# Kernel tuning notes

Measured on AMD Instinct MI355X. Metric: run time of the kernel, lower is better.

## Reference

```python
import jax, jax.numpy as jnp
import numpy as np

N = 65536      # nodes in batched graph
E = 2097152    # edges (avg degree 32)
V = 1000       # chord vocabulary size
F_IN = 128     # chord feature dim
H = 256        # hidden_dim
OUT = 128      # out_dim
G = 256        # number of graphs in batch


def _gcn_layer(x, W, b, row, col, norm, n):
    # x: [n, f_in] -> [n, f_out]; PyG GCNConv: linear then normalized aggregation + bias
    x = x @ W
    msg = x[row] * norm[:, None]            # gather at source, scale by sym-norm
    return jax.ops.segment_sum(msg, col, num_segments=n) + b


def setup_inputs() -> dict:
    key = jax.random.key(0)
    ks = jax.random.split(key, 9)
    chord_feats = jax.random.normal(ks[0], (V, F_IN), jnp.float32)
    W1 = jax.random.normal(ks[1], (F_IN, H), jnp.float32) * 0.05
    b1 = jnp.zeros((H,), jnp.float32)
    W2 = jax.random.normal(ks[2], (H, OUT), jnp.float32) * 0.05
    b2 = jnp.zeros((OUT,), jnp.float32)
    edge_attr = jax.random.uniform(ks[3], (E,), jnp.float32)          # positive edge weights
    node_indices = jax.random.randint(ks[4], (N,), 0, V, jnp.int64)
    edge_index = jax.random.randint(ks[5], (2, E), 0, N, jnp.int64)
    batch_index = jnp.sort(jax.random.randint(ks[6], (N,), 0, G, jnp.int64))
    return {"chord_feats": chord_feats, "W1": W1, "b1": b1, "W2": W2, "b2": b2,
            "edge_attr": edge_attr, "node_indices": node_indices,
            "edge_index": edge_index, "batch_index": batch_index}


def reference(chord_feats, W1, b1, W2, b2, edge_attr, node_indices, edge_index, batch_index):
    loops = jnp.arange(N, dtype=edge_index.dtype)
    row = jnp.concatenate([edge_index[0], loops])   # source
    col = jnp.concatenate([edge_index[1], loops])   # target
    ew = jnp.concatenate([edge_attr, jnp.ones((N,), edge_attr.dtype)])  # self-loop weight 1
    # symmetric GCN normalization: D^-1/2 A D^-1/2
    deg = jax.ops.segment_sum(ew, col, num_segments=N)
    dis = jnp.where(deg > 0, jax.lax.rsqrt(jnp.maximum(deg, 1e-30)), 0.0)
    norm = dis[row] * ew * dis[col]

    x = chord_feats[node_indices]                   # [N, F_IN]
    x = jax.nn.relu(_gcn_layer(x, W1, b1, row, col, norm, N))
    x = jax.nn.relu(_gcn_layer(x, W2, b2, row, col, norm, N))

    # global_mean_pool over batch_index
    sums = jax.ops.segment_sum(x, batch_index, num_segments=G)
    counts = jax.ops.segment_sum(jnp.ones((N,), x.dtype), batch_index, num_segments=G)
    return sums / jnp.maximum(counts, 1.0)[:, None]
```

## Files before the change

### kernel.cpp

```cpp
#include <hip/hip_runtime.h>
#include <hip/hip_fp16.h>
#include <math.h>

constexpr int N_NODES = 65536;
constexpr int N_EDGES = 2097152;
constexpr int F_IN    = 128;
constexpr int H_DIM   = 256;
constexpr int O_DIM   = 128;
constexpr int N_GRAPH = 256;
constexpr int V_SIZE  = 1000;

constexpr int EPB  = 8192;
constexpr int NBLK = N_EDGES / EPB;
constexpr float FXP = 16777216.0f;

typedef _Float16 half8 __attribute__((ext_vector_type(8)));
typedef float floatx4 __attribute__((ext_vector_type(4)));


__global__ void k_init(float* __restrict__ pool, const int* __restrict__ batch,
                       float* __restrict__ cntf, const float* __restrict__ cf,
                       const float* __restrict__ W1, __half* __restrict__ cfW1,
                       const float* __restrict__ W2, _Float16* __restrict__ W2T) {
    __shared__ float xs[8 * F_IN];
    int i = blockIdx.x * blockDim.x + threadIdx.x;
    if (i < N_GRAPH * O_DIM) pool[i] = 0.0f;
    if (blockIdx.x == 0) {
        int g = threadIdx.x;
        int lo = 0, hi = N_NODES;
        while (lo < hi) { int m = (lo + hi) >> 1; if (batch[m] < g) lo = m + 1; else hi = m; }
        int start = lo;
        lo = 0; hi = N_NODES;
        while (lo < hi) { int m = (lo + hi) >> 1; if (batch[m] <= g) lo = m + 1; else hi = m; }
        cntf[g] = (float)(lo - start);
    }
    if (blockIdx.x < V_SIZE / 8) {
        int rb = blockIdx.x * 8;
        int t  = threadIdx.x;
        #pragma unroll
        for (int p = 0; p < 4; ++p) {
            int idx = p * 256 + t;
            int r = idx >> 7, k = idx & 127;
            xs[idx] = cf[(size_t)(rb + r) * F_IN + k];
        }
        __syncthreads();
        float acc[8] = {};
        for (int k = 0; k < F_IN; ++k) {
            float w = W1[k * H_DIM + t];
            #pragma unroll
            for (int j = 0; j < 8; ++j) acc[j] += xs[j * F_IN + k] * w;
        }
        #pragma unroll
        for (int j = 0; j < 8; ++j)
            cfW1[(size_t)(rb + j) * H_DIM + t] = __float2half(acc[j]);
    }
    if (blockIdx.x >= 128) {
        int idx = (blockIdx.x - 128) * 256 + threadIdx.x;
        int nn = idx >> 8, kk = idx & 255;
        W2T[idx] = (_Float16)W2[kk * O_DIM + nn];
    }
}


__global__ void k_hist(const int* __restrict__ col, int* __restrict__ hist) {
    __shared__ int h[256];
    int t = threadIdx.x;
    h[t] = 0;
    __syncthreads();
    int base = blockIdx.x * EPB;
    #pragma unroll
    for (int i = 0; i < EPB / 256; ++i)
        atomicAdd(&h[col[base + i * 256 + t] >> 8], 1);
    __syncthreads();
    hist[t * NBLK + blockIdx.x] = h[t];
}


__global__ void k_scan1(const int* __restrict__ in, int* __restrict__ out,
                        int* __restrict__ bsum) {
    __shared__ int s[256];
    int tid = threadIdx.x;
    int i = blockIdx.x * 256 + tid;
    int v = in[i];
    s[tid] = v;
    __syncthreads();
    for (int d = 1; d < 256; d <<= 1) {
        int t = (tid >= d) ? s[tid - d] : 0;
        __syncthreads();
        s[tid] += t;
        __syncthreads();
    }
    out[i] = s[tid] - v;
    if (tid == 255) bsum[blockIdx.x] = s[255];
}

__global__ void k_scan2(int* __restrict__ bsum) {
    __shared__ int s[256];
    int tid = threadIdx.x;
    int v = bsum[tid];
    s[tid] = v;
    __syncthreads();
    for (int d = 1; d < 256; d <<= 1) {
        int t = (tid >= d) ? s[tid - d] : 0;
        __syncthreads();
        s[tid] += t;
        __syncthreads();
    }
    bsum[tid] = s[tid] - v;
}


__global__ void k_part(const int* __restrict__ row, const int* __restrict__ col,
                       const float* __restrict__ ew, const int* __restrict__ nidx,
                       const int* __restrict__ hoffs, const int* __restrict__ bsum,
                       int2* __restrict__ part) {
    __shared__ int cur[256];
    int t = threadIdx.x;
    cur[t] = hoffs[t * NBLK + blockIdx.x] + bsum[t];
    __syncthreads();
    int base = blockIdx.x * EPB;
    for (int i = 0; i < EPB / 256; ++i) {
        int e = base + i * 256 + t;
        int r = row[e], c = col[e];
        unsigned hw = (unsigned)__half_as_ushort(__float2half(ew[e]));
        int vb = nidx[r];
        int slot = atomicAdd(&cur[c >> 8], 1);
        int2 rec;
        rec.x = (r << 16) | ((c & 255) << 8) | (vb >> 2);
        rec.y = (int)(((unsigned)(vb & 3) << 16) | hw);
        part[slot] = rec;
    }
}


__global__ void k_build1(const int* __restrict__ hoffs, const int* __restrict__ bsum,
                         const int2* __restrict__ part, float* __restrict__ dis,
                         int* __restrict__ offs) {
    __shared__ unsigned long long dc[256];
    __shared__ int sc[256];
    int t = threadIdx.x;
    int bucket = blockIdx.x;
    dc[t] = 0ULL;
    __syncthreads();
    int start = hoffs[bucket * NBLK] + bsum[bucket];
    int end   = (bucket == 255) ? N_EDGES : (hoffs[(bucket + 1) * NBLK] + bsum[bucket + 1]);
    for (int j = start + t; j < end; j += 256) {
        int2 rec = part[j];
        int dst = (rec.x >> 8) & 255;
        float w = __half2float(__ushort_as_half((unsigned short)(rec.y & 0xFFFF)));
        atomicAdd(&dc[dst], (1ULL << 40) |
                  (unsigned long long)(unsigned)(w * FXP + 0.5f));
    }
    __syncthreads();
    unsigned long long v = dc[t];
    float deg = 1.0f + (float)(v & 0xFFFFFFFFFFULL) * (1.0f / FXP);
    dis[bucket * 256 + t] = 1.0f / sqrtf(deg);
    int cnt = (int)(v >> 40);
    sc[t] = cnt;
    __syncthreads();
    for (int d = 1; d < 256; d <<= 1) {
        int x = (t >= d) ? sc[t - d] : 0;
        __syncthreads();
        sc[t] += x;
        __syncthreads();
    }
    offs[bucket * 256 + t] = start + sc[t] - cnt;
    if (bucket == 255 && t == 255) offs[N_NODES] = N_EDGES;
}


__global__ void k_build2(const int* __restrict__ hoffs, const int* __restrict__ bsum,
                         const int2* __restrict__ part, const float* __restrict__ dis,
                         const int* __restrict__ offs, int2* __restrict__ csr) {
    __shared__ int cur[256];
    int t = threadIdx.x;
    int bucket = blockIdx.x;
    cur[t] = offs[bucket * 256 + t];
    __syncthreads();
    int start = hoffs[bucket * NBLK] + bsum[bucket];
    int end   = (bucket == 255) ? N_EDGES : (hoffs[(bucket + 1) * NBLK] + bsum[bucket + 1]);
    for (int j = start + t; j < end; j += 256) {
        int2 rec = part[j];
        int dst = (rec.x >> 8) & 255;
        unsigned src = ((unsigned)rec.x) >> 16;
        int vb = ((rec.x & 255) << 2) | ((rec.y >> 16) & 3);
        float w = __half2float(__ushort_as_half((unsigned short)(rec.y & 0xFFFF)));
        float nm = dis[src] * w;
        int slot = atomicAdd(&cur[dst], 1);
        int2 e;
        e.x = (int)((src << 10) | (unsigned)vb);
        e.y = __float_as_int(nm);
        csr[slot] = e;
    }
}

__device__ __forceinline__ void acc8(float* e, int4 v, float n) {
    float2 f0 = __half22float2(*(__half2*)&v.x);
    float2 f1 = __half22float2(*(__half2*)&v.y);
    float2 f2 = __half22float2(*(__half2*)&v.z);
    float2 f3 = __half22float2(*(__half2*)&v.w);
    e[0] += f0.x * n; e[1] += f0.y * n;
    e[2] += f1.x * n; e[3] += f1.y * n;
    e[4] += f2.x * n; e[5] += f2.y * n;
    e[6] += f3.x * n; e[7] += f3.y * n;
}


__global__ void k_agg1(const int4* __restrict__ cfW1, const int* __restrict__ nidx,
                       const float* __restrict__ dis, const int* __restrict__ offs,
                       const int2* __restrict__ csr, const float4* __restrict__ b1f4,
                       int4* __restrict__ h1) {
    int wave = threadIdx.x >> 6;
    int lane = threadIdx.x & 63;
    int g    = lane >> 5;
    int sl   = lane & 31;
    int c = blockIdx.x * 4 + wave;
    float d = dis[c];
    int4 sp = cfW1[(size_t)nidx[c] * 32 + sl];
    float esum[8] = {0.f, 0.f, 0.f, 0.f, 0.f, 0.f, 0.f, 0.f};
    int a0 = offs[c], a1 = offs[c + 1];
    int s = a0;
    if (s < a1 && (s & 1)) {
        int sb = __builtin_amdgcn_readfirstlane(s);
        int2 e0 = csr[sb];
        int4 v0 = cfW1[(size_t)(e0.x & 1023) * 32 + sl];
        float n = (g == 0) ? __int_as_float(e0.y) : 0.0f;
        acc8(esum, v0, n);
        ++s;
    }
    for (; s + 8 <= a1; s += 8) {
        int sb = __builtin_amdgcn_readfirstlane(s);
        int4 ee[4];
        #pragma unroll
        for (int u = 0; u < 4; ++u) ee[u] = *(const int4*)(csr + sb + 2 * u);
        int4 v[4]; float n[4];
        #pragma unroll
        for (int u = 0; u < 4; ++u) {
            int ex = g ? ee[u].z : ee[u].x;
            int ey = g ? ee[u].w : ee[u].y;
            n[u] = __int_as_float(ey);
            v[u] = cfW1[(size_t)(ex & 1023) * 32 + sl];
        }
        #pragma unroll
        for (int u = 0; u < 4; ++u) acc8(esum, v[u], n[u]);
    }
    for (; s + 2 <= a1; s += 2) {
        int sb = __builtin_amdgcn_readfirstlane(s);
        int4 ee = *(const int4*)(csr + sb);
        int ex = g ? ee.z : ee.x;
        int ey = g ? ee.w : ee.y;
        int4 v0 = cfW1[(size_t)(ex & 1023) * 32 + sl];
        acc8(esum, v0, __int_as_float(ey));
    }
    if (s < a1) {
        int sb = __builtin_amdgcn_readfirstlane(s);
        int2 e0 = csr[sb];
        int4 v0 = cfW1[(size_t)(e0.x & 1023) * 32 + sl];
        float n = (g == 0) ? __int_as_float(e0.y) : 0.0f;
        acc8(esum, v0, n);
    }
    #pragma unroll
    for (int k = 0; k < 8; ++k) esum[k] += __shfl_xor(esum[k], 32, 64);

    float dd = d * d;
    float2 s0 = __half22float2(*(__half2*)&sp.x);
    float2 s1 = __half22float2(*(__half2*)&sp.y);
    float2 s2 = __half22float2(*(__half2*)&sp.z);
    float2 s3 = __half22float2(*(__half2*)&sp.w);
    float4 bb0 = b1f4[2 * sl];
    float4 bb1 = b1f4[2 * sl + 1];
    float r[8];
    r[0] = bb0.x + s0.x * dd + d * esum[0];
    r[1] = bb0.y + s0.y * dd + d * esum[1];
    r[2] = bb0.z + s1.x * dd + d * esum[2];
    r[3] = bb0.w + s1.y * dd + d * esum[3];
    r[4] = bb1.x + s2.x * dd + d * esum[4];
    r[5] = bb1.y + s2.y * dd + d * esum[5];
    r[6] = bb1.z + s3.x * dd + d * esum[6];
    r[7] = bb1.w + s3.y * dd + d * esum[7];
    #pragma unroll
    for (int k = 0; k < 8; ++k) r[k] = r[k] > 0.f ? r[k] : 0.f;
    float2 p0 = {r[0], r[1]}, p1 = {r[2], r[3]}, p2 = {r[4], r[5]}, p3 = {r[6], r[7]};
    __half2 h0 = __float22half2_rn(p0);
    __half2 h1v = __float22half2_rn(p1);
    __half2 h2 = __float22half2_rn(p2);
    __half2 h3 = __float22half2_rn(p3);
    int4 outv;
    outv.x = *(int*)&h0;
    outv.y = *(int*)&h1v;
    outv.z = *(int*)&h2;
    outv.w = *(int*)&h3;
    if (lane < 32) h1[(size_t)c * 32 + sl] = outv;
}


__global__ void k_gemm2(const _Float16* __restrict__ h1, const _Float16* __restrict__ W2T,
                        __half* __restrict__ xw2h) {
    int wave = threadIdx.x >> 6;
    int lane = threadIdx.x & 63;
    int quad = lane >> 4;
    int n    = lane & 15;
    int tm   = blockIdx.x * 4 + wave;
    const _Float16* arow = h1 + (size_t)(tm * 16 + n) * H_DIM;
    half8 a[8];
    #pragma unroll
    for (int kt = 0; kt < 8; ++kt)
        a[kt] = *(const half8*)(arow + kt * 32 + quad * 8);
    #pragma unroll
    for (int nt = 0; nt < 8; ++nt) {
        floatx4 acc = {0.f, 0.f, 0.f, 0.f};
        const _Float16* brow = W2T + (size_t)(nt * 16 + n) * H_DIM;
        #pragma unroll
        for (int kt = 0; kt < 8; ++kt) {
            half8 b = *(const half8*)(brow + kt * 32 + quad * 8);
            acc = __builtin_amdgcn_mfma_f32_16x16x32_f16(a[kt], b, acc, 0, 0, 0);
        }
        #pragma unroll
        for (int r = 0; r < 4; ++r) {
            int rowi = tm * 16 + quad * 4 + r;
            xw2h[(size_t)rowi * O_DIM + nt * 16 + n] = __float2half(acc[r]);
        }
    }
}


__global__ void k_agg2_pool(const int4* __restrict__ xw2h, const float* __restrict__ b2,
                            const float* __restrict__ dis, const int* __restrict__ offs,
                            const int2* __restrict__ csr, const int* __restrict__ batch,
                            float* __restrict__ pool) {
    __shared__ float red[4][128];
    __shared__ int bgs[4];
    int wave = threadIdx.x >> 6;
    int lane = threadIdx.x & 63;
    int grp  = lane >> 4;
    int sl   = lane & 15;
    int c = blockIdx.x * 4 + wave;
    float d = dis[c];
    int4 sp = xw2h[(size_t)c * 16 + sl];
    float esum[8] = {0.f, 0.f, 0.f, 0.f, 0.f, 0.f, 0.f, 0.f};
    int s0 = offs[c], s1 = offs[c + 1];
    int s = s0;
    for (; s + 16 <= s1; s += 16) {
        int sb = __builtin_amdgcn_readfirstlane(s);
        int2 e[4];
        #pragma unroll
        for (int u = 0; u < 4; ++u) e[u] = csr[sb + 4 * u + grp];
        int4 v[4];
        #pragma unroll
        for (int u = 0; u < 4; ++u)
            v[u] = xw2h[(size_t)(((unsigned)e[u].x) >> 10) * 16 + sl];
        #pragma unroll
        for (int u = 0; u < 4; ++u) acc8(esum, v[u], __int_as_float(e[u].y));
    }
    for (; s + 4 <= s1; s += 4) {
        int sb = __builtin_amdgcn_readfirstlane(s);
        int2 e0 = csr[sb + grp];
        int4 v0 = xw2h[(size_t)(((unsigned)e0.x) >> 10) * 16 + sl];
        acc8(esum, v0, __int_as_float(e0.y));
    }
    if (s < s1) {
        int sb = __builtin_amdgcn_readfirstlane(s);
        int idx = sb + grp;
        int idc = idx < s1 ? idx : s1 - 1;
        int2 e0 = csr[idc];
        int4 v0 = xw2h[(size_t)(((unsigned)e0.x) >> 10) * 16 + sl];
        float n = (idx < s1) ? __int_as_float(e0.y) : 0.0f;
        acc8(esum, v0, n);
    }
    #pragma unroll
    for (int k = 0; k < 8; ++k) {
        esum[k] += __shfl_xor(esum[k], 16, 64);
        esum[k] += __shfl_xor(esum[k], 32, 64);
    }
    float dd = d * d;
    float2 f0 = __half22float2(*(__half2*)&sp.x);
    float2 f1 = __half22float2(*(__half2*)&sp.y);
    float2 f2 = __half22float2(*(__half2*)&sp.z);
    float2 f3 = __half22float2(*(__half2*)&sp.w);
    float4 bb0 = ((const float4*)b2)[2 * sl];
    float4 bb1 = ((const float4*)b2)[2 * sl + 1];
    float acc[8];
    acc[0] = bb0.x + f0.x * dd + d * esum[0];
    acc[1] = bb0.y + f0.y * dd + d * esum[1];
    acc[2] = bb0.z + f1.x * dd + d * esum[2];
    acc[3] = bb0.w + f1.y * dd + d * esum[3];
    acc[4] = bb1.x + f2.x * dd + d * esum[4];
    acc[5] = bb1.y + f2.y * dd + d * esum[5];
    acc[6] = bb1.z + f3.x * dd + d * esum[6];
    acc[7] = bb1.w + f3.y * dd + d * esum[7];
    #pragma unroll
    for (int k = 0; k < 8; ++k) acc[k] = acc[k] > 0.f ? acc[k] : 0.f;
    if (grp == 0) {
        #pragma unroll
        for (int k = 0; k < 8; ++k) red[wave][8 * sl + k] = acc[k];
    }
    if (lane == 0) bgs[wave] = batch[c];
    __syncthreads();
    if (wave == 0) {
        float2 a;
        a.x = red[0][2 * lane];
        a.y = red[0][2 * lane + 1];
        int cg = bgs[0];
        #pragma unroll
        for (int w = 1; w < 4; ++w) {
            int g = bgs[w];
            float2 r;
            r.x = red[w][2 * lane];
            r.y = red[w][2 * lane + 1];
            if (g == cg) { a.x += r.x; a.y += r.y; }
            else {
                atomicAdd(&pool[cg * O_DIM + 2 * lane], a.x);
                atomicAdd(&pool[cg * O_DIM + 2 * lane + 1], a.y);
                a = r; cg = g;
            }
        }
        atomicAdd(&pool[cg * O_DIM + 2 * lane], a.x);
        atomicAdd(&pool[cg * O_DIM + 2 * lane + 1], a.y);
    }
}

__global__ void k_final(const float* __restrict__ pool, const float* __restrict__ cnt,
                        float* __restrict__ out) {
    int t = blockIdx.x * blockDim.x + threadIdx.x;
    if (t < N_GRAPH * O_DIM) {
        int g = t / O_DIM;
        out[t] = pool[t] / fmaxf(cnt[g], 1.0f);
    }
}


extern "C" void kernel_launch(void* const* d_in, const int* in_sizes, int n_in,
                              void* d_out, int out_size, void* d_ws, size_t ws_size,
                              hipStream_t stream) {
    const float* cf   = (const float*)d_in[0];
    const float* W1   = (const float*)d_in[1];
    const float* b1   = (const float*)d_in[2];
    const float* W2   = (const float*)d_in[3];
    const float* b2   = (const float*)d_in[4];
    const float* ew   = (const float*)d_in[5];
    const int*   nidx = (const int*)d_in[6];
    const int*   eidx = (const int*)d_in[7];
    const int*   bidx = (const int*)d_in[8];
    float* out = (float*)d_out;

    const int* row = eidx;
    const int* col = eidx + N_EDGES;

    char* ws = (char*)d_ws;
    size_t off = 0;
    int*   hist  = (int*)  (ws + off); off += (size_t)N_NODES * 4;
    int*   hoffs = (int*)  (ws + off); off += (size_t)N_NODES * 4;
    int*   bsum  = (int*)  (ws + off); off += 4096;
    float* dis   = (float*)(ws + off); off += (size_t)N_NODES * 4;
    int*   offs  = (int*)  (ws + off); off += (size_t)(N_NODES + 16) * 4;
    int2*  csr   = (int2*) (ws + off); off += (size_t)N_EDGES * 8;
    float* pool  = (float*)(ws + off); off += (size_t)(N_GRAPH * O_DIM + N_GRAPH) * 4;
    __half* cfW1 = (__half*)(ws + off); off += (size_t)V_SIZE * H_DIM * 2;
    _Float16* W2T = (_Float16*)(ws + off); off += (size_t)O_DIM * H_DIM * 2;
    off = (off + 255) & ~(size_t)255;
    int2*  part  = (int2*) (ws + off); off += (size_t)N_EDGES * 8;
    __half* h1   = (__half*)(ws + off);
    __half* xw2h = (__half*)part;
    float* cntf  = pool + N_GRAPH * O_DIM;

    k_init<<<256, 256, 0, stream>>>(pool, bidx, cntf, cf, W1, cfW1, W2, W2T);
    k_hist<<<NBLK, 256, 0, stream>>>(col, hist);
    k_scan1<<<256, 256, 0, stream>>>(hist, hoffs, bsum);
    k_scan2<<<1, 256, 0, stream>>>(bsum);

    k_part<<<NBLK, 256, 0, stream>>>(row, col, ew, nidx, hoffs, bsum, part);
    k_build1<<<256, 256, 0, stream>>>(hoffs, bsum, part, dis, offs);
    k_build2<<<256, 256, 0, stream>>>(hoffs, bsum, part, dis, offs, csr);

    k_agg1<<<N_NODES / 4, 256, 0, stream>>>((const int4*)cfW1, nidx, dis, offs, csr,
                                            (const float4*)b1, (int4*)h1);

    k_gemm2<<<N_NODES / 64, 256, 0, stream>>>((const _Float16*)h1, W2T, xw2h);
    k_agg2_pool<<<N_NODES / 4, 256, 0, stream>>>((const int4*)xw2h, b2, dis, offs, csr,
                                                 bidx, pool);

    k_final<<<(N_GRAPH * O_DIM + 255) / 256, 256, 0, stream>>>(pool, cntf, out);
}
```

Measured before the change: 331.5 us.

## Split layer-2 aggregation into four feature-slice passes with sliced xw2h layout

The GEMM2 output is stored as four column slices of 32 halves per node, and the aggregation-plus-pool kernel runs four passes, each gathering only a 64-byte slice per neighbor with 16 edges handled per wave step. The aim is to shrink each pass's gather working set so it fits better in cache and gives better locality for random neighbor reads. The cost is reading the CSR edge list four times, plus more cross-lane shuffles and more pool atomics. CSR loads are marked nontemporal so these repeated streams do not evict the feature slices.

```diff
diff --git a/kernel.cpp b/kernel.cpp
--- a/kernel.cpp
+++ b/kernel.cpp
@@ -318,7 +318,9 @@
         #pragma unroll
         for (int r = 0; r < 4; ++r) {
             int rowi = tm * 16 + quad * 4 + r;
-            xw2h[(size_t)rowi * O_DIM + nt * 16 + n] = __float2half(acc[r]);
+            int dgl = nt * 16 + n;
+            xw2h[(size_t)(dgl >> 5) * ((size_t)N_NODES * 32)
+                 + (size_t)rowi * 32 + (dgl & 31)] = __float2half(acc[r]);
         }
     }
 }
@@ -328,94 +330,94 @@
                             const float* __restrict__ dis, const int* __restrict__ offs,
                             const int2* __restrict__ csr, const int* __restrict__ batch,
                             float* __restrict__ pool) {
-    __shared__ float red[4][128];
+    __shared__ float red[4][32];
     __shared__ int bgs[4];
     int wave = threadIdx.x >> 6;
     int lane = threadIdx.x & 63;
-    int grp  = lane >> 4;
-    int sl   = lane & 15;
-    int c = blockIdx.x * 4 + wave;
+    int grp  = lane >> 2;
+    int sl   = lane & 3;
+    int pass = blockIdx.x >> 14;
+    int c    = (blockIdx.x & 16383) * 4 + wave;
+    const int4* t = xw2h + (size_t)pass * N_NODES * 4;
     float d = dis[c];
-    int4 sp = xw2h[(size_t)c * 16 + sl];
+    int4 sp = t[(size_t)c * 4 + sl];
     float esum[8] = {0.f, 0.f, 0.f, 0.f, 0.f, 0.f, 0.f, 0.f};
     int s0 = offs[c], s1 = offs[c + 1];
     int s = s0;
+    for (; s + 32 <= s1; s += 32) {
+        int sb = __builtin_amdgcn_readfirstlane(s);
+        long long r0 = __builtin_nontemporal_load((const long long*)(csr + sb + grp));
+        long long r1 = __builtin_nontemporal_load((const long long*)(csr + sb + 16 + grp));
+        int2 e0 = *(int2*)&r0;
+        int2 e1 = *(int2*)&r1;
+        int4 v0 = t[(size_t)(((unsigned)e0.x) >> 10) * 4 + sl];
+        int4 v1 = t[(size_t)(((unsigned)e1.x) >> 10) * 4 + sl];
+        acc8(esum, v0, __int_as_float(e0.y));
+        acc8(esum, v1, __int_as_float(e1.y));
+    }
     for (; s + 16 <= s1; s += 16) {
         int sb = __builtin_amdgcn_readfirstlane(s);
-        int2 e[4];
-        #pragma unroll
-        for (int u = 0; u < 4; ++u) e[u] = csr[sb + 4 * u + grp];
-        int4 v[4];
-        #pragma unroll
-        for (int u = 0; u < 4; ++u)
-            v[u] = xw2h[(size_t)(((unsigned)e[u].x) >> 10) * 16 + sl];
-        #pragma unroll
-        for (int u = 0; u < 4; ++u) acc8(esum, v[u], __int_as_float(e[u].y));
-    }
-    for (; s + 4 <= s1; s += 4) {
-        int sb = __builtin_amdgcn_readfirstlane(s);
-        int2 e0 = csr[sb + grp];
-        int4 v0 = xw2h[(size_t)(((unsigned)e0.x) >> 10) * 16 + sl];
+        long long r0 = __builtin_nontemporal_load((const long long*)(csr + sb + grp));
+        int2 e0 = *(int2*)&r0;
+        int4 v0 = t[(size_t)(((unsigned)e0.x) >> 10) * 4 + sl];
         acc8(esum, v0, __int_as_float(e0.y));
     }
     if (s < s1) {
         int sb = __builtin_amdgcn_readfirstlane(s);
         int idx = sb + grp;
         int idc = idx < s1 ? idx : s1 - 1;
-        int2 e0 = csr[idc];
-        int4 v0 = xw2h[(size_t)(((unsigned)e0.x) >> 10) * 16 + sl];
+        long long r0 = __builtin_nontemporal_load((const long long*)(csr + idc));
+        int2 e0 = *(int2*)&r0;
+        int4 v0 = t[(size_t)(((unsigned)e0.x) >> 10) * 4 + sl];
         float n = (idx < s1) ? __int_as_float(e0.y) : 0.0f;
         acc8(esum, v0, n);
     }
     #pragma unroll
     for (int k = 0; k < 8; ++k) {
+        esum[k] += __shfl_xor(esum[k], 4, 64);
+        esum[k] += __shfl_xor(esum[k], 8, 64);
         esum[k] += __shfl_xor(esum[k], 16, 64);
         esum[k] += __shfl_xor(esum[k], 32, 64);
     }
-    float dd = d * d;
-    float2 f0 = __half22float2(*(__half2*)&sp.x);
-    float2 f1 = __half22float2(*(__half2*)&sp.y);
-    float2 f2 = __half22float2(*(__half2*)&sp.z);
-    float2 f3 = __half22float2(*(__half2*)&sp.w);
-    float4 bb0 = ((const float4*)b2)[2 * sl];
-    float4 bb1 = ((const float4*)b2)[2 * sl + 1];
-    float acc[8];
-    acc[0] = bb0.x + f0.x * dd + d * esum[0];
-    acc[1] = bb0.y + f0.y * dd + d * esum[1];
-    acc[2] = bb0.z + f1.x * dd + d * esum[2];
-    acc[3] = bb0.w + f1.y * dd + d * esum[3];
-    acc[4] = bb1.x + f2.x * dd + d * esum[4];
-    acc[5] = bb1.y + f2.y * dd + d * esum[5];
-    acc[6] = bb1.z + f3.x * dd + d * esum[6];
-    acc[7] = bb1.w + f3.y * dd + d * esum[7];
-    #pragma unroll
-    for (int k = 0; k < 8; ++k) acc[k] = acc[k] > 0.f ? acc[k] : 0.f;
     if (grp == 0) {
-        #pragma unroll
-        for (int k = 0; k < 8; ++k) red[wave][8 * sl + k] = acc[k];
+        float dd = d * d;
+        float2 f0 = __half22float2(*(__half2*)&sp.x);
+        float2 f1 = __half22float2(*(__half2*)&sp.y);
+        float2 f2 = __half22float2(*(__half2*)&sp.z);
+        float2 f3 = __half22float2(*(__half2*)&sp.w);
+        float4 bb0 = ((const float4*)b2)[pass * 8 + sl * 2];
+        float4 bb1 = ((const float4*)b2)[pass * 8 + sl * 2 + 1];
+        float acc[8];
+        acc[0] = bb0.x + f0.x * dd + d * esum[0];
+        acc[1] = bb0.y + f0.y * dd + d * esum[1];
+        acc[2] = bb0.z + f1.x * dd + d * esum[2];
+        acc[3] = bb0.w + f1.y * dd + d * esum[3];
+        acc[4] = bb1.x + f2.x * dd + d * esum[4];
+        acc[5] = bb1.y + f2.y * dd + d * esum[5];
+        acc[6] = bb1.z + f3.x * dd + d * esum[6];
+        acc[7] = bb1.w + f3.y * dd + d * esum[7];
+        #pragma unroll
+        for (int k = 0; k < 8; ++k) {
+            float v = acc[k] > 0.f ? acc[k] : 0.f;
+            red[wave][sl * 8 + k] = v;
+        }
     }
     if (lane == 0) bgs[wave] = batch[c];
     __syncthreads();
-    if (wave == 0) {
-        float2 a;
-        a.x = red[0][2 * lane];
-        a.y = red[0][2 * lane + 1];
+    if (wave == 0 && lane < 32) {
+        float a = red[0][lane];
         int cg = bgs[0];
         #pragma unroll
         for (int w = 1; w < 4; ++w) {
             int g = bgs[w];
-            float2 r;
-            r.x = red[w][2 * lane];
-            r.y = red[w][2 * lane + 1];
-            if (g == cg) { a.x += r.x; a.y += r.y; }
+            float r = red[w][lane];
+            if (g == cg) { a += r; }
             else {
-                atomicAdd(&pool[cg * O_DIM + 2 * lane], a.x);
-                atomicAdd(&pool[cg * O_DIM + 2 * lane + 1], a.y);
+                atomicAdd(&pool[cg * O_DIM + pass * 32 + lane], a);
                 a = r; cg = g;
             }
         }
-        atomicAdd(&pool[cg * O_DIM + 2 * lane], a.x);
-        atomicAdd(&pool[cg * O_DIM + 2 * lane + 1], a.y);
+        atomicAdd(&pool[cg * O_DIM + pass * 32 + lane], a);
     }
 }
 
@@ -476,8 +478,8 @@
                                             (const float4*)b1, (int4*)h1);
 
     k_gemm2<<<N_NODES / 64, 256, 0, stream>>>((const _Float16*)h1, W2T, xw2h);
-    k_agg2_pool<<<N_NODES / 4, 256, 0, stream>>>((const int4*)xw2h, b2, dis, offs, csr,
-                                                 bidx, pool);
+    k_agg2_pool<<<4 * (N_NODES / 4), 256, 0, stream>>>((const int4*)xw2h, b2, dis, offs,
+                                                       csr, bidx, pool);
 
     k_final<<<(N_GRAPH * O_DIM + 255) / 256, 256, 0, stream>>>(pool, cntf, out);
 }
```

Measured after the change: 390.1 us. +17.7%, slower.

## Fuse layer-1 aggregation with layer-2 GEMM via LDS; deepen agg2 unroll

Applied to the files above, without the earlier changes.

Merges the layer-1 aggregation kernel and the layer-2 MFMA GEMM into one kernel. Each block aggregates 16 nodes into an LDS tile and then multiplies that tile by W2T, with each wave covering two output column tiles. This removes the global h1 write and reread and one kernel launch. The trade-off is that each wave now handles 4 nodes serially and the grid is 4x smaller, which may reduce latency hiding. Separately, the agg2 edge loop is unrolled from 16 to 32 edges with nontemporal CSR loads, to put more loads in flight.

```diff
diff --git a/kernel.cpp b/kernel.cpp
--- a/kernel.cpp
+++ b/kernel.cpp
@@ -206,108 +206,110 @@
 }
 
 
-__global__ void k_agg1(const int4* __restrict__ cfW1, const int* __restrict__ nidx,
-                       const float* __restrict__ dis, const int* __restrict__ offs,
-                       const int2* __restrict__ csr, const float4* __restrict__ b1f4,
-                       int4* __restrict__ h1) {
+__global__ void __launch_bounds__(256) k_agg1g2(
+        const int4* __restrict__ cfW1, const int* __restrict__ nidx,
+        const float* __restrict__ dis, const int* __restrict__ offs,
+        const int2* __restrict__ csr, const float4* __restrict__ b1f4,
+        const _Float16* __restrict__ W2T, __half* __restrict__ xw2h) {
+    __shared__ _Float16 h1s[16 * 264];
     int wave = threadIdx.x >> 6;
     int lane = threadIdx.x & 63;
     int g    = lane >> 5;
     int sl   = lane & 31;
-    int c = blockIdx.x * 4 + wave;
-    float d = dis[c];
-    int4 sp = cfW1[(size_t)nidx[c] * 32 + sl];
-    float esum[8] = {0.f, 0.f, 0.f, 0.f, 0.f, 0.f, 0.f, 0.f};
-    int a0 = offs[c], a1 = offs[c + 1];
-    int s = a0;
-    if (s < a1 && (s & 1)) {
-        int sb = __builtin_amdgcn_readfirstlane(s);
-        int2 e0 = csr[sb];
-        int4 v0 = cfW1[(size_t)(e0.x & 1023) * 32 + sl];
-        float n = (g == 0) ? __int_as_float(e0.y) : 0.0f;
-        acc8(esum, v0, n);
-        ++s;
-    }
-    for (; s + 8 <= a1; s += 8) {
-        int sb = __builtin_amdgcn_readfirstlane(s);
-        int4 ee[4];
-        #pragma unroll
-        for (int u = 0; u < 4; ++u) ee[u] = *(const int4*)(csr + sb + 2 * u);
-        int4 v[4]; float n[4];
-        #pragma unroll
-        for (int u = 0; u < 4; ++u) {
-            int ex = g ? ee[u].z : ee[u].x;
-            int ey = g ? ee[u].w : ee[u].y;
-            n[u] = __int_as_float(ey);
-            v[u] = cfW1[(size_t)(ex & 1023) * 32 + sl];
-        }
-        #pragma unroll
-        for (int u = 0; u < 4; ++u) acc8(esum, v[u], n[u]);
-    }
-    for (; s + 2 <= a1; s += 2) {
-        int sb = __builtin_amdgcn_readfirstlane(s);
-        int4 ee = *(const int4*)(csr + sb);
-        int ex = g ? ee.z : ee.x;
-        int ey = g ? ee.w : ee.y;
-        int4 v0 = cfW1[(size_t)(ex & 1023) * 32 + sl];
-        acc8(esum, v0, __int_as_float(ey));
-    }
-    if (s < a1) {
-        int sb = __builtin_amdgcn_readfirstlane(s);
-        int2 e0 = csr[sb];
-        int4 v0 = cfW1[(size_t)(e0.x & 1023) * 32 + sl];
-        float n = (g == 0) ? __int_as_float(e0.y) : 0.0f;
-        acc8(esum, v0, n);
-    }
-    #pragma unroll
-    for (int k = 0; k < 8; ++k) esum[k] += __shfl_xor(esum[k], 32, 64);
-
-    float dd = d * d;
-    float2 s0 = __half22float2(*(__half2*)&sp.x);
-    float2 s1 = __half22float2(*(__half2*)&sp.y);
-    float2 s2 = __half22float2(*(__half2*)&sp.z);
-    float2 s3 = __half22float2(*(__half2*)&sp.w);
+    int rowbase = blockIdx.x * 16;
+
     float4 bb0 = b1f4[2 * sl];
     float4 bb1 = b1f4[2 * sl + 1];
-    float r[8];
-    r[0] = bb0.x + s0.x * dd + d * esum[0];
-    r[1] = bb0.y + s0.y * dd + d * esum[1];
-    r[2] = bb0.z + s1.x * dd + d * esum[2];
-    r[3] = bb0.w + s1.y * dd + d * esum[3];
-    r[4] = bb1.x + s2.x * dd + d * esum[4];
-    r[5] = bb1.y + s2.y * dd + d * esum[5];
-    r[6] = bb1.z + s3.x * dd + d * esum[6];
-    r[7] = bb1.w + s3.y * dd + d * esum[7];
-    #pragma unroll
-    for (int k = 0; k < 8; ++k) r[k] = r[k] > 0.f ? r[k] : 0.f;
-    float2 p0 = {r[0], r[1]}, p1 = {r[2], r[3]}, p2 = {r[4], r[5]}, p3 = {r[6], r[7]};
-    __half2 h0 = __float22half2_rn(p0);
-    __half2 h1v = __float22half2_rn(p1);
-    __half2 h2 = __float22half2_rn(p2);
-    __half2 h3 = __float22half2_rn(p3);
-    int4 outv;
-    outv.x = *(int*)&h0;
-    outv.y = *(int*)&h1v;
-    outv.z = *(int*)&h2;
-    outv.w = *(int*)&h3;
-    if (lane < 32) h1[(size_t)c * 32 + sl] = outv;
-}
-
-
-__global__ void k_gemm2(const _Float16* __restrict__ h1, const _Float16* __restrict__ W2T,
-                        __half* __restrict__ xw2h) {
-    int wave = threadIdx.x >> 6;
-    int lane = threadIdx.x & 63;
+
+    for (int j = 0; j < 4; ++j) {
+        int c = rowbase + wave * 4 + j;
+        float d = dis[c];
+        int4 sp = cfW1[(size_t)nidx[c] * 32 + sl];
+        float esum[8] = {0.f, 0.f, 0.f, 0.f, 0.f, 0.f, 0.f, 0.f};
+        int a0 = offs[c], a1 = offs[c + 1];
+        int s = a0;
+        if (s < a1 && (s & 1)) {
+            int sb = __builtin_amdgcn_readfirstlane(s);
+            int2 e0 = csr[sb];
+            int4 v0 = cfW1[(size_t)(e0.x & 1023) * 32 + sl];
+            float n = (g == 0) ? __int_as_float(e0.y) : 0.0f;
+            acc8(esum, v0, n);
+            ++s;
+        }
+        for (; s + 8 <= a1; s += 8) {
+            int sb = __builtin_amdgcn_readfirstlane(s);
+            int4 ee[4];
+            #pragma unroll
+            for (int u = 0; u < 4; ++u) ee[u] = *(const int4*)(csr + sb + 2 * u);
+            int4 v[4]; float n[4];
+            #pragma unroll
+            for (int u = 0; u < 4; ++u) {
+                int ex = g ? ee[u].z : ee[u].x;
+                int ey = g ? ee[u].w : ee[u].y;
+                n[u] = __int_as_float(ey);
+                v[u] = cfW1[(size_t)(ex & 1023) * 32 + sl];
+            }
+            #pragma unroll
+            for (int u = 0; u < 4; ++u) acc8(esum, v[u], n[u]);
+        }
+        for (; s + 2 <= a1; s += 2) {
+            int sb = __builtin_amdgcn_readfirstlane(s);
+            int4 ee = *(const int4*)(csr + sb);
+            int ex = g ? ee.z : ee.x;
+            int ey = g ? ee.w : ee.y;
+            int4 v0 = cfW1[(size_t)(ex & 1023) * 32 + sl];
+            acc8(esum, v0, __int_as_float(ey));
+        }
+        if (s < a1) {
+            int sb = __builtin_amdgcn_readfirstlane(s);
+            int2 e0 = csr[sb];
+            int4 v0 = cfW1[(size_t)(e0.x & 1023) * 32 + sl];
+            float n = (g == 0) ? __int_as_float(e0.y) : 0.0f;
+            acc8(esum, v0, n);
+        }
+        #pragma unroll
+        for (int k = 0; k < 8; ++k) esum[k] += __shfl_xor(esum[k], 32, 64);
+
+        float dd = d * d;
+        float2 s0 = __half22float2(*(__half2*)&sp.x);
+        float2 s1 = __half22float2(*(__half2*)&sp.y);
+        float2 s2 = __half22float2(*(__half2*)&sp.z);
+        float2 s3 = __half22float2(*(__half2*)&sp.w);
+        float r[8];
+        r[0] = bb0.x + s0.x * dd + d * esum[0];
+        r[1] = bb0.y + s0.y * dd + d * esum[1];
+        r[2] = bb0.z + s1.x * dd + d * esum[2];
+        r[3] = bb0.w + s1.y * dd + d * esum[3];
+        r[4] = bb1.x + s2.x * dd + d * esum[4];
+        r[5] = bb1.y + s2.y * dd + d * esum[5];
+        r[6] = bb1.z + s3.x * dd + d * esum[6];
+        r[7] = bb1.w + s3.y * dd + d * esum[7];
+        #pragma unroll
+        for (int k = 0; k < 8; ++k) r[k] = r[k] > 0.f ? r[k] : 0.f;
+        float2 p0 = {r[0], r[1]}, p1 = {r[2], r[3]}, p2 = {r[4], r[5]}, p3 = {r[6], r[7]};
+        __half2 h0 = __float22half2_rn(p0);
+        __half2 h1v = __float22half2_rn(p1);
+        __half2 h2 = __float22half2_rn(p2);
+        __half2 h3 = __float22half2_rn(p3);
+        int4 outv;
+        outv.x = *(int*)&h0;
+        outv.y = *(int*)&h1v;
+        outv.z = *(int*)&h2;
+        outv.w = *(int*)&h3;
+        if (lane < 32)
+            *(int4*)&h1s[(wave * 4 + j) * 264 + sl * 8] = outv;
+    }
+    __syncthreads();
+
     int quad = lane >> 4;
     int n    = lane & 15;
-    int tm   = blockIdx.x * 4 + wave;
-    const _Float16* arow = h1 + (size_t)(tm * 16 + n) * H_DIM;
     half8 a[8];
     #pragma unroll
     for (int kt = 0; kt < 8; ++kt)
-        a[kt] = *(const half8*)(arow + kt * 32 + quad * 8);
+        a[kt] = *(const half8*)&h1s[n * 264 + kt * 32 + quad * 8];
     #pragma unroll
-    for (int nt = 0; nt < 8; ++nt) {
+    for (int t2 = 0; t2 < 2; ++t2) {
+        int nt = wave * 2 + t2;
         floatx4 acc = {0.f, 0.f, 0.f, 0.f};
         const _Float16* brow = W2T + (size_t)(nt * 16 + n) * H_DIM;
         #pragma unroll
@@ -317,7 +319,7 @@
         }
         #pragma unroll
         for (int r = 0; r < 4; ++r) {
-            int rowi = tm * 16 + quad * 4 + r;
+            int rowi = rowbase + quad * 4 + r;
             xw2h[(size_t)rowi * O_DIM + nt * 16 + n] = __float2half(acc[r]);
         }
     }
@@ -340,17 +342,20 @@
     float esum[8] = {0.f, 0.f, 0.f, 0.f, 0.f, 0.f, 0.f, 0.f};
     int s0 = offs[c], s1 = offs[c + 1];
     int s = s0;
-    for (; s + 16 <= s1; s += 16) {
+    for (; s + 32 <= s1; s += 32) {
         int sb = __builtin_amdgcn_readfirstlane(s);
-        int2 e[4];
-        #pragma unroll
-        for (int u = 0; u < 4; ++u) e[u] = csr[sb + 4 * u + grp];
-        int4 v[4];
-        #pragma unroll
-        for (int u = 0; u < 4; ++u)
+        int2 e[8];
+        #pragma unroll
+        for (int u = 0; u < 8; ++u) {
+            long long rr = __builtin_nontemporal_load((const long long*)(csr + sb + 4 * u + grp));
+            e[u] = *(int2*)&rr;
+        }
+        int4 v[8];
+        #pragma unroll
+        for (int u = 0; u < 8; ++u)
             v[u] = xw2h[(size_t)(((unsigned)e[u].x) >> 10) * 16 + sl];
         #pragma unroll
-        for (int u = 0; u < 4; ++u) acc8(esum, v[u], __int_as_float(e[u].y));
+        for (int u = 0; u < 8; ++u) acc8(esum, v[u], __int_as_float(e[u].y));
     }
     for (; s + 4 <= s1; s += 4) {
         int sb = __builtin_amdgcn_readfirstlane(s);
@@ -459,7 +464,6 @@
     _Float16* W2T = (_Float16*)(ws + off); off += (size_t)O_DIM * H_DIM * 2;
     off = (off + 255) & ~(size_t)255;
     int2*  part  = (int2*) (ws + off); off += (size_t)N_EDGES * 8;
-    __half* h1   = (__half*)(ws + off);
     __half* xw2h = (__half*)part;
     float* cntf  = pool + N_GRAPH * O_DIM;
 
@@ -472,10 +476,9 @@
     k_build1<<<256, 256, 0, stream>>>(hoffs, bsum, part, dis, offs);
     k_build2<<<256, 256, 0, stream>>>(hoffs, bsum, part, dis, offs, csr);
 
-    k_agg1<<<N_NODES / 4, 256, 0, stream>>>((const int4*)cfW1, nidx, dis, offs, csr,
-                                            (const float4*)b1, (int4*)h1);
-
-    k_gemm2<<<N_NODES / 64, 256, 0, stream>>>((const _Float16*)h1, W2T, xw2h);
+    k_agg1g2<<<N_NODES / 16, 256, 0, stream>>>((const int4*)cfW1, nidx, dis, offs, csr,
+                                               (const float4*)b1, W2T, xw2h);
+
     k_agg2_pool<<<N_NODES / 4, 256, 0, stream>>>((const int4*)xw2h, b2, dis, offs, csr,
                                                  bidx, pool);
 
```

Result: slower. 374.1 us (+12.8%).
